# Kernel tuning notes

Measured on AMD Instinct MI355X. Metric: run time of the kernel, lower is better.

## Reference

```python
import jax, jax.numpy as jnp
import numpy as np

B, NQ, S, D = 2, 2048, 2048, 1024
H, HD, OUT = 16, 64, 1024


def setup_inputs() -> dict:
    key = jax.random.key(0)
    ks = jax.random.split(key, 8)
    scale = 1.0 / np.sqrt(D)
    return {
        "queries": jax.random.normal(ks[0], (B, NQ, D), jnp.float32),
        "keys": jax.random.normal(ks[1], (B, S, D), jnp.float32),
        "values": jax.random.normal(ks[2], (B, S, D), jnp.float32),
        "indicators": jax.random.uniform(ks[3], (B, S), jnp.float32),
        "Wq": jax.random.normal(ks[4], (D, H * HD), jnp.float32) * scale,
        "Wk": jax.random.normal(ks[5], (D, H * HD), jnp.float32) * scale,
        "Wv": jax.random.normal(ks[6], (D, H * HD), jnp.float32) * scale,
        "Wo": jax.random.normal(ks[7], (H * HD, OUT), jnp.float32) * scale,
    }


def reference(queries, keys, values, indicators, Wq, Wk, Wv, Wo):
    b, nq, _ = queries.shape
    s = keys.shape[1]
    # projections -> [b, len, H, HD] -> [b, H, len, HD]
    Q = (queries @ Wq).reshape(b, nq, H, HD).transpose(0, 2, 1, 3)
    K = (keys @ Wk).reshape(b, s, H, HD).transpose(0, 2, 1, 3)
    V = (values @ Wv).reshape(b, s, H, HD).transpose(0, 2, 1, 3)
    # scores [b, H, nq, s], softmax over s, THEN multiplicative mask
    scores = jnp.einsum("bhqd,bhkd->bhqk", Q, K) / jnp.sqrt(jnp.float32(HD))
    probs = jax.nn.softmax(scores, axis=-1)
    probs = probs * indicators[:, None, None, :]  # post-softmax mask
    ctx = jnp.einsum("bhqk,bhkd->bhqd", probs, V)
    ctx = ctx.transpose(0, 2, 1, 3).reshape(b, nq, H * HD)
    return ctx @ Wo
```

## Files before the change

kernel.cpp:

```cpp
#include <hip/hip_runtime.h>


typedef float f32x4 __attribute__((ext_vector_type(4)));
typedef __bf16 bf16x8 __attribute__((ext_vector_type(8)));
typedef __bf16 bf16x4 __attribute__((ext_vector_type(4)));

#define DEVINL __device__ __forceinline__

DEVINL void gll16(const void* g, void* l) {
  __builtin_amdgcn_global_load_lds((const __attribute__((address_space(1))) void*)g,
                                   (__attribute__((address_space(3))) void*)l, 16, 0, 0);
}
DEVINL bf16x8 ldfrag(const void* p) { return __builtin_bit_cast(bf16x8, *(const int4*)p); }
DEVINL f32x4 mfma16(bf16x8 a, bf16x8 b, f32x4 c) {
  return __builtin_amdgcn_mfma_f32_16x16x32_bf16(a, b, c, 0, 0, 0);
}
DEVINL unsigned cvtpk(float a, float b) {
  union {
    __bf16 h[2];
    unsigned u;
  } r;
  r.h[0] = (__bf16)a;
  r.h[1] = (__bf16)b;
  return r.u;
}
DEVINL void swap32(unsigned& a, unsigned& b) {
  asm("v_permlane32_swap_b32 %0, %1" : "+v"(a), "+v"(b));
}
DEVINL void swap16(unsigned& a, unsigned& b) {
  asm("v_permlane16_swap_b32 %0, %1" : "+v"(a), "+v"(b));
}

__global__ __launch_bounds__(256) void prep_k(
    const float* __restrict__ q, const float* __restrict__ k,
    const float* __restrict__ v, const float* __restrict__ Wq,
    const float* __restrict__ Wk, const float* __restrict__ Wv,
    const float* __restrict__ Wo, __bf16* __restrict__ qo, __bf16* __restrict__ ko,
    __bf16* __restrict__ vo, __bf16* __restrict__ o0, __bf16* __restrict__ o1,
    __bf16* __restrict__ o2, __bf16* __restrict__ o3) {
  const int bid = blockIdx.x;
  const int t = threadIdx.x;
  if (bid < 12288) {
    int plane = bid >> 12, bx = bid & 4095;
    const float* s = plane == 0 ? q : (plane == 1 ? k : v);
    __bf16* d = plane == 0 ? qo : (plane == 1 ? ko : vo);
    size_t i = ((size_t)bx * 256 + t) * 4;
    float4 f = *(const float4*)(s + i);
    bf16x4 o = {(__bf16)f.x, (__bf16)f.y, (__bf16)f.z, (__bf16)f.w};
    *(bf16x4*)(d + i) = o;
  } else {
    __shared__ float tl[32][33];
    int wid = bid - 12288;
    int z = wid >> 10, x = wid & 31, y = (wid >> 5) & 31;
    const float* W = z == 0 ? Wq : z == 1 ? Wk : z == 2 ? Wv : Wo;
    __bf16* o = z == 0 ? o0 : z == 1 ? o1 : z == 2 ? o2 : o3;
    float scale = z == 0 ? 0.125f * 1.44269504f : 1.0f;
    int c0 = x * 32, r0 = y * 32;
    int tx = t & 31, ty = t >> 5;
#pragma unroll
    for (int rr = 0; rr < 32; rr += 8)
      tl[rr + ty][tx] = W[(size_t)(r0 + rr + ty) * 1024 + c0 + tx];
    __syncthreads();
#pragma unroll
    for (int cc = 0; cc < 32; cc += 8)
      o[(size_t)(c0 + cc + ty) * 1024 + r0 + tx] = (__bf16)(tl[tx][cc + ty] * scale);
  }
}

template <int MT>
DEVINL void gemm_core(const __bf16* __restrict__ A, const __bf16* __restrict__ Bt,
                      int K, int m0, int n0, char* As, char* Bs, f32x4 (&acc)[MT][4],
                      int t) {
  const int lane = t & 63, wv = t >> 6;
  const int li = lane & 15, g = lane >> 4;
  const int wr = wv >> 1, wc = wv & 1;
  const size_t lda = (size_t)K * 2;
  for (int kt = 0; kt < K; kt += 32) {
    if (kt) __syncthreads();
#pragma unroll
    for (int p = 0; p < MT / 2; ++p) {
      int off = p * 4096 + t * 16;
      int row = off >> 6, ch = (off >> 4) & 3;
      int gch = ch ^ ((row >> 1) & 3);
      gll16((const char*)A + (size_t)(m0 + row) * lda + (size_t)kt * 2 + gch * 16,
            As + off);
    }
#pragma unroll
    for (int p = 0; p < 2; ++p) {
      int off = p * 4096 + t * 16;
      int row = off >> 6, ch = (off >> 4) & 3;
      int gch = ch ^ ((row >> 1) & 3);
      gll16((const char*)Bt + (size_t)(n0 + row) * lda + (size_t)kt * 2 + gch * 16,
            Bs + off);
    }
    __syncthreads();
    bf16x8 af[MT], bfr[4];
#pragma unroll
    for (int mt = 0; mt < MT; ++mt) {
      int row = wr * (MT * 16) + mt * 16 + li;
      int gch = g ^ ((row >> 1) & 3);
      af[mt] = ldfrag(As + row * 64 + gch * 16);
    }
#pragma unroll
    for (int nt = 0; nt < 4; ++nt) {
      int row = wc * 64 + nt * 16 + li;
      int gch = g ^ ((row >> 1) & 3);
      bfr[nt] = ldfrag(Bs + row * 64 + gch * 16);
    }
#pragma unroll
    for (int mt = 0; mt < MT; ++mt)
#pragma unroll
      for (int nt = 0; nt < 4; ++nt)
        acc[mt][nt] = mfma16(af[mt], bfr[nt], acc[mt][nt]);
  }
}

__global__ __launch_bounds__(256) void gemm_qkv(
    const __bf16* __restrict__ qb, const __bf16* __restrict__ kb,
    const __bf16* __restrict__ vb, const __bf16* __restrict__ WqT,
    const __bf16* __restrict__ WkT, const __bf16* __restrict__ WvT,
    const float* __restrict__ ind, __bf16* __restrict__ Qp, __bf16* __restrict__ Kp,
    __bf16* __restrict__ Vtp) {
  __shared__ __align__(16) char As[4 * 2048];
  __shared__ __align__(16) char Bs[8192];
  const int z = blockIdx.z;
  const __bf16* A = z == 0 ? qb : z == 1 ? kb : vb;
  const __bf16* Bt = z == 0 ? WqT : z == 1 ? WkT : WvT;
  const int m0 = blockIdx.y * 128, n0 = blockIdx.x * 128;
  f32x4 acc[4][4] = {};
  gemm_core<4>(A, Bt, 1024, m0, n0, As, Bs, acc, threadIdx.x);
  const int lane = threadIdx.x & 63, wv = threadIdx.x >> 6;
  const int li = lane & 15, g = lane >> 4;
  const int wr = wv >> 1, wc = wv & 1;
#pragma unroll
  for (int mt = 0; mt < 4; ++mt)
#pragma unroll
    for (int nt = 0; nt < 4; ++nt) {
      int m = m0 + wr * 64 + mt * 16 + g * 4;
      int n = n0 + wc * 64 + nt * 16 + li;
      if (z < 2) {
        __bf16* Cb = z ? Kp : Qp;
#pragma unroll
        for (int r = 0; r < 4; ++r)
          Cb[(size_t)(m + r) * 1024 + n] = (__bf16)acc[mt][nt][r];
      } else {
        float4 i4 = *(const float4*)(ind + m);
        bf16x4 o = {(__bf16)(acc[mt][nt][0] * i4.x), (__bf16)(acc[mt][nt][1] * i4.y),
                    (__bf16)(acc[mt][nt][2] * i4.z), (__bf16)(acc[mt][nt][3] * i4.w)};
        *(bf16x4*)(Vtp + (size_t)n * 4096 + m) = o;
      }
    }
}

__global__ __launch_bounds__(256) void gemm_out(const __bf16* __restrict__ ctx,
                                                const __bf16* __restrict__ WoT,
                                                float* __restrict__ out) {
  __shared__ __align__(16) char As[2 * 2048];
  __shared__ __align__(16) char Bs[8192];
  const int m0 = blockIdx.y * 64, n0 = blockIdx.x * 128;
  f32x4 acc[2][4] = {};
  gemm_core<2>(ctx, WoT, 1024, m0, n0, As, Bs, acc, threadIdx.x);
  const int lane = threadIdx.x & 63, wv = threadIdx.x >> 6;
  const int li = lane & 15, g = lane >> 4;
  const int wr = wv >> 1, wc = wv & 1;
#pragma unroll
  for (int mt = 0; mt < 2; ++mt)
#pragma unroll
    for (int nt = 0; nt < 4; ++nt) {
      int m = m0 + wr * 32 + mt * 16 + g * 4;
      int n = n0 + wc * 64 + nt * 16 + li;
#pragma unroll
      for (int r = 0; r < 4; ++r) out[(size_t)(m + r) * 1024 + n] = acc[mt][nt][r];
    }
}

__global__ __launch_bounds__(256) void flash_k(
    const __bf16* __restrict__ Qp, const __bf16* __restrict__ Kp,
    const __bf16* __restrict__ Vt, __bf16* __restrict__ ctx0,
    __bf16* __restrict__ ctx1, __bf16* __restrict__ ctx2, float* __restrict__ pl) {
  __shared__ __align__(16) char smem[16384];
  char* kv = smem;
  const int t = threadIdx.x;
  const int lane = t & 63, wv = t >> 6;
  const int li = lane & 15, g = lane >> 4;
  const int sp = blockIdx.x >> 9, rest = blockIdx.x & 511;
  const int qt = rest & 15, h = (rest >> 4) & 15, b = rest >> 8;
  const int kt0 = (sp * 32) / 3, kt1 = (sp * 32 + 32) / 3;
  const size_t qrow0 = (size_t)b * 2048 + (size_t)qt * 128;
  __bf16* ctx = sp == 0 ? ctx0 : (sp == 1 ? ctx1 : ctx2);

#pragma unroll
  for (int p = 0; p < 4; ++p) {
    int off = p * 4096 + t * 16;
    int row = off >> 7, ch = (off >> 4) & 7;
    int gch = ch ^ (row & 7);
    gll16((const char*)Qp + ((qrow0 + row) * 1024 + h * 64) * 2 + gch * 16, smem + off);
  }
  __syncthreads();

  bf16x8 qf[2][2];
#pragma unroll
  for (int nt = 0; nt < 2; ++nt)
#pragma unroll
    for (int ks = 0; ks < 2; ++ks) {
      int row = wv * 32 + nt * 16 + li;
      int gch = (4 * ks + g) ^ (row & 7);
      qf[nt][ks] = ldfrag(smem + row * 128 + gch * 16);
    }

  f32x4 acc[4][2] = {};
  float lsum[2] = {0.0f, 0.0f};

  for (int kt = kt0; kt < kt1; ++kt) {
    __syncthreads();
#pragma unroll
    for (int p = 0; p < 2; ++p) {
      int off = p * 4096 + t * 16;
      int row = off >> 7, ch = (off >> 4) & 7;
      int gch = ch ^ (row & 7);
      gll16((const char*)Kp +
                (((size_t)b * 2048 + kt * 64 + row) * 1024 + h * 64) * 2 + gch * 16,
            kv + off);
      gll16((const char*)Vt +
                ((size_t)(h * 64 + row) * 4096 + (size_t)b * 2048 + kt * 64) * 2 +
                gch * 16,
            kv + 8192 + off);
    }
    __syncthreads();

    unsigned pk[4][2][2];
#pragma unroll
    for (int mt = 0; mt < 4; ++mt) {
      f32x4 st0 = {}, st1 = {};
      int row = mt * 16 + li;
#pragma unroll
      for (int ks = 0; ks < 2; ++ks) {
        int gch = (4 * ks + g) ^ (row & 7);
        bf16x8 kf = ldfrag(kv + row * 128 + gch * 16);
        st0 = mfma16(kf, qf[0][ks], st0);
        st1 = mfma16(kf, qf[1][ks], st1);
      }
      float p0 = __builtin_amdgcn_exp2f(st0[0]);
      float p1 = __builtin_amdgcn_exp2f(st0[1]);
      float p2 = __builtin_amdgcn_exp2f(st0[2]);
      float p3 = __builtin_amdgcn_exp2f(st0[3]);
      lsum[0] += (p0 + p1) + (p2 + p3);
      pk[mt][0][0] = cvtpk(p0, p1);
      pk[mt][0][1] = cvtpk(p2, p3);
      p0 = __builtin_amdgcn_exp2f(st1[0]);
      p1 = __builtin_amdgcn_exp2f(st1[1]);
      p2 = __builtin_amdgcn_exp2f(st1[2]);
      p3 = __builtin_amdgcn_exp2f(st1[3]);
      lsum[1] += (p0 + p1) + (p2 + p3);
      pk[mt][1][0] = cvtpk(p0, p1);
      pk[mt][1][1] = cvtpk(p2, p3);
    }

#pragma unroll
    for (int kc = 0; kc < 2; ++kc) {
      unsigned a00 = pk[2 * kc][0][0], b00 = pk[2 * kc + 1][0][0];
      unsigned a01 = pk[2 * kc][0][1], b01 = pk[2 * kc + 1][0][1];
      unsigned a10 = pk[2 * kc][1][0], b10 = pk[2 * kc + 1][1][0];
      unsigned a11 = pk[2 * kc][1][1], b11 = pk[2 * kc + 1][1][1];
      swap32(a00, b00);
      swap16(a00, b00);
      swap32(a01, b01);
      swap16(a01, b01);
      swap32(a10, b10);
      swap16(a10, b10);
      swap32(a11, b11);
      swap16(a11, b11);
      uint4 u0 = {a00, a01, b00, b01};
      uint4 u1 = {a10, a11, b10, b11};
      bf16x8 pf0 = __builtin_bit_cast(bf16x8, u0);
      bf16x8 pf1 = __builtin_bit_cast(bf16x8, u1);
#pragma unroll
      for (int mtd = 0; mtd < 4; ++mtd) {
        int row = mtd * 16 + li;
        int gch = (4 * kc + g) ^ (row & 7);
        bf16x8 vf = ldfrag(kv + 8192 + row * 128 + gch * 16);
        acc[mtd][0] = mfma16(vf, pf0, acc[mtd][0]);
        acc[mtd][1] = mfma16(vf, pf1, acc[mtd][1]);
      }
    }
  }

#pragma unroll
  for (int nt = 0; nt < 2; ++nt) {
    float l = lsum[nt];
    l += __shfl_xor(l, 16);
    l += __shfl_xor(l, 32);
    float linv = 1.0f / l;
    size_t qrow = qrow0 + wv * 32 + nt * 16 + li;
    if (g == 0) pl[((size_t)sp * 4096 + qrow) * 16 + h] = l;
#pragma unroll
    for (int mtd = 0; mtd < 4; ++mtd) {
      bf16x4 o = {(__bf16)(acc[mtd][nt][0] * linv), (__bf16)(acc[mtd][nt][1] * linv),
                  (__bf16)(acc[mtd][nt][2] * linv), (__bf16)(acc[mtd][nt][3] * linv)};
      *(bf16x4*)(ctx + qrow * 1024 + h * 64 + mtd * 16 + g * 4) = o;
    }
  }
}

__global__ __launch_bounds__(256) void combine_k(const __bf16* __restrict__ c0,
                                                 const __bf16* __restrict__ c1,
                                                 const __bf16* __restrict__ c2,
                                                 const float* __restrict__ pl,
                                                 __bf16* __restrict__ ctx) {
  size_t e = ((size_t)blockIdx.x * 256 + threadIdx.x) * 8;
  int qrow = (int)(e >> 10), h = ((int)e & 1023) >> 6;
  float l0 = pl[(size_t)qrow * 16 + h];
  float l1 = pl[(size_t)(4096 + qrow) * 16 + h];
  float l2 = pl[(size_t)(8192 + qrow) * 16 + h];
  float w = 1.0f / (l0 + l1 + l2);
  float w0 = l0 * w, w1 = l1 * w, w2 = l2 * w;
  bf16x8 a = *(const bf16x8*)(c0 + e);
  bf16x8 b = *(const bf16x8*)(c1 + e);
  bf16x8 c = *(const bf16x8*)(c2 + e);
  bf16x8 o;
#pragma unroll
  for (int i = 0; i < 8; ++i)
    o[i] = (__bf16)((float)a[i] * w0 + (float)b[i] * w1 + (float)c[i] * w2);
  *(bf16x8*)(ctx + e) = o;
}

extern "C" void kernel_launch(void* const* d_in, const int* in_sizes, int n_in,
                              void* d_out, int out_size, void* d_ws, size_t ws_size,
                              hipStream_t stream) {
  const float* q = (const float*)d_in[0];
  const float* k = (const float*)d_in[1];
  const float* v = (const float*)d_in[2];
  const float* ind = (const float*)d_in[3];
  const float* Wq = (const float*)d_in[4];
  const float* Wk = (const float*)d_in[5];
  const float* Wv = (const float*)d_in[6];
  const float* Wo = (const float*)d_in[7];
  char* ws = (char*)d_ws;
  const size_t MB = 1024 * 1024;
  __bf16* qb = (__bf16*)(ws + 0);
  __bf16* kb = (__bf16*)(ws + 8 * MB);
  __bf16* vb = (__bf16*)(ws + 16 * MB);
  __bf16* WqT = (__bf16*)(ws + 24 * MB);
  __bf16* WkT = (__bf16*)(ws + 26 * MB);
  __bf16* WvT = (__bf16*)(ws + 28 * MB);
  __bf16* WoT = (__bf16*)(ws + 30 * MB);
  __bf16* Qp = (__bf16*)(ws + 32 * MB);
  __bf16* Kp = (__bf16*)(ws + 40 * MB);
  __bf16* Vtp = (__bf16*)(ws + 48 * MB);
  __bf16* ctx0 = (__bf16*)(ws + 0);
  __bf16* ctx1 = (__bf16*)(ws + 8 * MB);
  __bf16* ctx2 = (__bf16*)(ws + 16 * MB);
  float* pl = (float*)(ws + 24 * MB);
  __bf16* ctx = (__bf16*)(ws + 48 * MB);
  float* out = (float*)d_out;

  prep_k<<<dim3(16384), 256, 0, stream>>>(q, k, v, Wq, Wk, Wv, Wo, qb, kb, vb, WqT,
                                          WkT, WvT, WoT);
  gemm_qkv<<<dim3(8, 32, 3), 256, 0, stream>>>(qb, kb, vb, WqT, WkT, WvT, ind, Qp, Kp,
                                               Vtp);
  flash_k<<<dim3(1536), 256, 0, stream>>>(Qp, Kp, Vtp, ctx0, ctx1, ctx2, pl);
  combine_k<<<dim3(2048), 256, 0, stream>>>(ctx0, ctx1, ctx2, pl, ctx);
  gemm_out<<<dim3(8, 64), 256, 0, stream>>>(ctx, WoT, out);
}
```

Measured before the change: 228.2 us.

## Double-buffer K tiles and split K/V waits in flash attention loop

Restructures the flash attention inner loop so the next K tile is prefetched into a second LDS buffer while the current one is consumed. V loads are issued at the start of each iteration and waited on only before the PV MFMAs, using explicit vmcnt waits and raw barriers instead of __syncthreads. It also raises wave priority around the MFMA sections. The aim is to hide global-to-LDS latency behind the QK and softmax compute, at the cost of 8KB more LDS and fragile hand-counted waitcnt ordering.

```diff
diff --git a/kernel.cpp b/kernel.cpp
--- a/kernel.cpp
+++ b/kernel.cpp
@@ -30,6 +30,11 @@
 DEVINL void swap16(unsigned& a, unsigned& b) {
   asm("v_permlane16_swap_b32 %0, %1" : "+v"(a), "+v"(b));
 }
+
+#define SBAR() __builtin_amdgcn_s_barrier()
+#define SCHED0() __builtin_amdgcn_sched_barrier(0)
+#define WAITV(n) asm volatile("s_waitcnt vmcnt(" #n ")" ::: "memory")
+#define WAITL0() asm volatile("s_waitcnt lgkmcnt(0)" ::: "memory")
 
 __global__ __launch_bounds__(256) void prep_k(
     const float* __restrict__ q, const float* __restrict__ k,
@@ -178,14 +183,15 @@
     const __bf16* __restrict__ Qp, const __bf16* __restrict__ Kp,
     const __bf16* __restrict__ Vt, __bf16* __restrict__ ctx0,
     __bf16* __restrict__ ctx1, __bf16* __restrict__ ctx2, float* __restrict__ pl) {
-  __shared__ __align__(16) char smem[16384];
-  char* kv = smem;
+  __shared__ __align__(16) char smem[24576];
+  char* vbuf = smem + 16384;
   const int t = threadIdx.x;
   const int lane = t & 63, wv = t >> 6;
   const int li = lane & 15, g = lane >> 4;
   const int sp = blockIdx.x >> 9, rest = blockIdx.x & 511;
   const int qt = rest & 15, h = (rest >> 4) & 15, b = rest >> 8;
   const int kt0 = (sp * 32) / 3, kt1 = (sp * 32 + 32) / 3;
+  const int ntile = kt1 - kt0;
   const size_t qrow0 = (size_t)b * 2048 + (size_t)qt * 128;
   __bf16* ctx = sp == 0 ? ctx0 : (sp == 1 ? ctx1 : ctx2);
 
@@ -194,9 +200,21 @@
     int off = p * 4096 + t * 16;
     int row = off >> 7, ch = (off >> 4) & 7;
     int gch = ch ^ (row & 7);
-    gll16((const char*)Qp + ((qrow0 + row) * 1024 + h * 64) * 2 + gch * 16, smem + off);
-  }
-  __syncthreads();
+    gll16((const char*)Qp + ((qrow0 + row) * 1024 + h * 64) * 2 + gch * 16,
+          smem + 8192 + off);
+  }
+#pragma unroll
+  for (int p = 0; p < 2; ++p) {
+    int off = p * 4096 + t * 16;
+    int row = off >> 7, ch = (off >> 4) & 7;
+    int gch = ch ^ (row & 7);
+    gll16((const char*)Kp +
+              (((size_t)b * 2048 + kt0 * 64 + row) * 1024 + h * 64) * 2 + gch * 16,
+          smem + off);
+  }
+  WAITV(2);
+  SBAR();
+  SCHED0();
 
   bf16x8 qf[2][2];
 #pragma unroll
@@ -205,30 +223,50 @@
     for (int ks = 0; ks < 2; ++ks) {
       int row = wv * 32 + nt * 16 + li;
       int gch = (4 * ks + g) ^ (row & 7);
-      qf[nt][ks] = ldfrag(smem + row * 128 + gch * 16);
-    }
+      qf[nt][ks] = ldfrag(smem + 8192 + row * 128 + gch * 16);
+    }
+  SCHED0();
+  WAITL0();
+  SBAR();
+  SCHED0();
 
   f32x4 acc[4][2] = {};
   float lsum[2] = {0.0f, 0.0f};
 
-  for (int kt = kt0; kt < kt1; ++kt) {
-    __syncthreads();
+  for (int t_ = 0; t_ < ntile; ++t_) {
+    const int kt = kt0 + t_;
+    char* kbuf = smem + (t_ & 1) * 8192;
 #pragma unroll
     for (int p = 0; p < 2; ++p) {
       int off = p * 4096 + t * 16;
       int row = off >> 7, ch = (off >> 4) & 7;
       int gch = ch ^ (row & 7);
-      gll16((const char*)Kp +
-                (((size_t)b * 2048 + kt * 64 + row) * 1024 + h * 64) * 2 + gch * 16,
-            kv + off);
       gll16((const char*)Vt +
                 ((size_t)(h * 64 + row) * 4096 + (size_t)b * 2048 + kt * 64) * 2 +
                 gch * 16,
-            kv + 8192 + off);
-    }
-    __syncthreads();
+            vbuf + off);
+    }
+    if (t_ + 1 < ntile) {
+      char* knxt = smem + ((t_ + 1) & 1) * 8192;
+#pragma unroll
+      for (int p = 0; p < 2; ++p) {
+        int off = p * 4096 + t * 16;
+        int row = off >> 7, ch = (off >> 4) & 7;
+        int gch = ch ^ (row & 7);
+        gll16((const char*)Kp +
+                  (((size_t)b * 2048 + (kt + 1) * 64 + row) * 1024 + h * 64) * 2 +
+                  gch * 16,
+              knxt + off);
+      }
+      WAITV(4);
+    } else {
+      WAITV(2);
+    }
+    SBAR();
+    SCHED0();
 
     unsigned pk[4][2][2];
+    __builtin_amdgcn_s_setprio(1);
 #pragma unroll
     for (int mt = 0; mt < 4; ++mt) {
       f32x4 st0 = {}, st1 = {};
@@ -236,7 +274,7 @@
 #pragma unroll
       for (int ks = 0; ks < 2; ++ks) {
         int gch = (4 * ks + g) ^ (row & 7);
-        bf16x8 kf = ldfrag(kv + row * 128 + gch * 16);
+        bf16x8 kf = ldfrag(kbuf + row * 128 + gch * 16);
         st0 = mfma16(kf, qf[0][ks], st0);
         st1 = mfma16(kf, qf[1][ks], st1);
       }
@@ -255,7 +293,18 @@
       pk[mt][1][0] = cvtpk(p0, p1);
       pk[mt][1][1] = cvtpk(p2, p3);
     }
-
+    __builtin_amdgcn_s_setprio(0);
+
+    SCHED0();
+    if (t_ + 1 < ntile) {
+      WAITV(2);
+    } else {
+      WAITV(0);
+    }
+    SBAR();
+    SCHED0();
+
+    __builtin_amdgcn_s_setprio(1);
 #pragma unroll
     for (int kc = 0; kc < 2; ++kc) {
       unsigned a00 = pk[2 * kc][0][0], b00 = pk[2 * kc + 1][0][0];
@@ -278,11 +327,17 @@
       for (int mtd = 0; mtd < 4; ++mtd) {
         int row = mtd * 16 + li;
         int gch = (4 * kc + g) ^ (row & 7);
-        bf16x8 vf = ldfrag(kv + 8192 + row * 128 + gch * 16);
+        bf16x8 vf = ldfrag(vbuf + row * 128 + gch * 16);
         acc[mtd][0] = mfma16(vf, pf0, acc[mtd][0]);
         acc[mtd][1] = mfma16(vf, pf1, acc[mtd][1]);
       }
     }
+    __builtin_amdgcn_s_setprio(0);
+
+    SCHED0();
+    WAITL0();
+    SBAR();
+    SCHED0();
   }
 
 #pragma unroll
```

Result: no change. 230.7 us (+1.1%).

## Stage transposed V output through LDS and remap GEMM block order

Applied to the files above, without the earlier changes.

The V projection epilogue now writes its masked bf16 tile into a padded shared-memory buffer and then emits coalesced 16-byte rows to the transposed Vt layout, replacing scattered 8-byte stores. Both the QKV and output GEMMs also remap the linear block index so consecutive blocks walk differently over M/N tiles, intended to spread work across XCDs and improve cache reuse. The shared buffer grows to about 34KB, which may reduce occupancy, and extra barriers are added in the V path.

```diff
diff --git a/kernel.cpp b/kernel.cpp
--- a/kernel.cpp
+++ b/kernel.cpp
@@ -121,35 +121,56 @@
     const __bf16* __restrict__ WkT, const __bf16* __restrict__ WvT,
     const float* __restrict__ ind, __bf16* __restrict__ Qp, __bf16* __restrict__ Kp,
     __bf16* __restrict__ Vtp) {
-  __shared__ __align__(16) char As[4 * 2048];
-  __shared__ __align__(16) char Bs[8192];
+  __shared__ __align__(16) char shm[34816];
+  char* As = shm;
+  char* Bs = shm + 8192;
   const int z = blockIdx.z;
   const __bf16* A = z == 0 ? qb : z == 1 ? kb : vb;
   const __bf16* Bt = z == 0 ? WqT : z == 1 ? WkT : WvT;
-  const int m0 = blockIdx.y * 128, n0 = blockIdx.x * 128;
+  const int lin = blockIdx.x + (int)blockIdx.y * 8;
+  const int w = (lin & 7) * 32 + (lin >> 3);
+  const int m0 = (w >> 3) * 128, n0 = (w & 7) * 128;
   f32x4 acc[4][4] = {};
   gemm_core<4>(A, Bt, 1024, m0, n0, As, Bs, acc, threadIdx.x);
   const int lane = threadIdx.x & 63, wv = threadIdx.x >> 6;
   const int li = lane & 15, g = lane >> 4;
   const int wr = wv >> 1, wc = wv & 1;
-#pragma unroll
-  for (int mt = 0; mt < 4; ++mt)
-#pragma unroll
-    for (int nt = 0; nt < 4; ++nt) {
-      int m = m0 + wr * 64 + mt * 16 + g * 4;
-      int n = n0 + wc * 64 + nt * 16 + li;
-      if (z < 2) {
-        __bf16* Cb = z ? Kp : Qp;
+  if (z < 2) {
+    __bf16* Cb = z ? Kp : Qp;
+#pragma unroll
+    for (int mt = 0; mt < 4; ++mt)
+#pragma unroll
+      for (int nt = 0; nt < 4; ++nt) {
+        int m = m0 + wr * 64 + mt * 16 + g * 4;
+        int n = n0 + wc * 64 + nt * 16 + li;
 #pragma unroll
         for (int r = 0; r < 4; ++r)
           Cb[(size_t)(m + r) * 1024 + n] = (__bf16)acc[mt][nt][r];
-      } else {
+      }
+  } else {
+    __syncthreads();
+    __bf16(*T)[136] = (__bf16(*)[136])shm;
+#pragma unroll
+    for (int mt = 0; mt < 4; ++mt)
+#pragma unroll
+      for (int nt = 0; nt < 4; ++nt) {
+        int m = m0 + wr * 64 + mt * 16 + g * 4;
+        int n_l = wc * 64 + nt * 16 + li;
         float4 i4 = *(const float4*)(ind + m);
         bf16x4 o = {(__bf16)(acc[mt][nt][0] * i4.x), (__bf16)(acc[mt][nt][1] * i4.y),
                     (__bf16)(acc[mt][nt][2] * i4.z), (__bf16)(acc[mt][nt][3] * i4.w)};
-        *(bf16x4*)(Vtp + (size_t)n * 4096 + m) = o;
+        *(bf16x4*)&T[n_l][wr * 64 + mt * 16 + g * 4] = o;
       }
-    }
+    __syncthreads();
+    const int tt = threadIdx.x;
+#pragma unroll
+    for (int pass = 0; pass < 8; ++pass) {
+      int n_l = pass * 16 + (tt >> 4);
+      int mc = (tt & 15) * 8;
+      int4 val = *(const int4*)&T[n_l][mc];
+      *(int4*)(Vtp + (size_t)(n0 + n_l) * 4096 + m0 + mc) = val;
+    }
+  }
 }
 
 __global__ __launch_bounds__(256) void gemm_out(const __bf16* __restrict__ ctx,
@@ -157,7 +178,9 @@
                                                 float* __restrict__ out) {
   __shared__ __align__(16) char As[2 * 2048];
   __shared__ __align__(16) char Bs[8192];
-  const int m0 = blockIdx.y * 64, n0 = blockIdx.x * 128;
+  const int lin = blockIdx.x + (int)blockIdx.y * 8;
+  const int w = (lin & 7) * 64 + (lin >> 3);
+  const int m0 = (w >> 3) * 64, n0 = (w & 7) * 128;
   f32x4 acc[2][4] = {};
   gemm_core<2>(ctx, WoT, 1024, m0, n0, As, Bs, acc, threadIdx.x);
   const int lane = threadIdx.x & 63, wv = threadIdx.x >> 6;
```

After: 233.6 us. 1.02x slower.

## Fuse split-KV combine into output projection GEMM A-tile load

Applied to the files above, without the earlier changes.

Removes the separate combine kernel and instead merges the three partial flash-attention context buffers, weighted by their softmax sums, while loading the A tile inside the output GEMM. This eliminates one launch and the write and re-read of the combined context buffer. In exchange, each column block of the output GEMM re-reads all three partial buffers and recomputes the weights. The A loads become synchronous register loads rather than async global-to-LDS copies.

```diff
diff --git a/kernel.cpp b/kernel.cpp
--- a/kernel.cpp
+++ b/kernel.cpp
@@ -152,17 +152,70 @@
     }
 }
 
-__global__ __launch_bounds__(256) void gemm_out(const __bf16* __restrict__ ctx,
-                                                const __bf16* __restrict__ WoT,
-                                                float* __restrict__ out) {
-  __shared__ __align__(16) char As[2 * 2048];
+__global__ __launch_bounds__(256) void gemm_out(
+    const __bf16* __restrict__ c0, const __bf16* __restrict__ c1,
+    const __bf16* __restrict__ c2, const float* __restrict__ pl,
+    const __bf16* __restrict__ WoT, float* __restrict__ out) {
+  __shared__ __align__(16) char As[4096];
   __shared__ __align__(16) char Bs[8192];
-  const int m0 = blockIdx.y * 64, n0 = blockIdx.x * 128;
-  f32x4 acc[2][4] = {};
-  gemm_core<2>(ctx, WoT, 1024, m0, n0, As, Bs, acc, threadIdx.x);
-  const int lane = threadIdx.x & 63, wv = threadIdx.x >> 6;
+  const int t = threadIdx.x;
+  const int lane = t & 63, wv = t >> 6;
   const int li = lane & 15, g = lane >> 4;
   const int wr = wv >> 1, wc = wv & 1;
+  const int m0 = blockIdx.y * 64, n0 = blockIdx.x * 128;
+  const int arow = t >> 2;
+  const int agch = (t & 3) ^ ((arow >> 1) & 3);
+  const size_t abase = (size_t)(m0 + arow) * 1024 + agch * 8;
+  const float* plr = pl + (size_t)(m0 + arow) * 16;
+  f32x4 acc[2][4] = {};
+  for (int kt = 0; kt < 32; ++kt) {
+    if (kt) __syncthreads();
+    {
+      const int h = kt >> 1;
+      float l0 = plr[h], l1 = plr[65536 + h], l2 = plr[131072 + h];
+      float w = 1.0f / (l0 + l1 + l2);
+      float w0 = l0 * w, w1 = l1 * w, w2 = l2 * w;
+      bf16x8 a = *(const bf16x8*)(c0 + abase + kt * 32);
+      bf16x8 b = *(const bf16x8*)(c1 + abase + kt * 32);
+      bf16x8 c = *(const bf16x8*)(c2 + abase + kt * 32);
+      unsigned ow[4];
+#pragma unroll
+      for (int i = 0; i < 4; ++i) {
+        float e0 = (float)a[2 * i] * w0 + (float)b[2 * i] * w1 + (float)c[2 * i] * w2;
+        float e1 = (float)a[2 * i + 1] * w0 + (float)b[2 * i + 1] * w1 +
+                   (float)c[2 * i + 1] * w2;
+        ow[i] = cvtpk(e0, e1);
+      }
+      *(int4*)(As + t * 16) = (int4){(int)ow[0], (int)ow[1], (int)ow[2], (int)ow[3]};
+    }
+#pragma unroll
+    for (int p = 0; p < 2; ++p) {
+      int off = p * 4096 + t * 16;
+      int row = off >> 6, ch = (off >> 4) & 3;
+      int gch = ch ^ ((row >> 1) & 3);
+      gll16((const char*)WoT + (size_t)(n0 + row) * 2048 + (size_t)kt * 64 + gch * 16,
+            Bs + off);
+    }
+    __syncthreads();
+    bf16x8 af[2], bfr[4];
+#pragma unroll
+    for (int mt = 0; mt < 2; ++mt) {
+      int row = wr * 32 + mt * 16 + li;
+      int gch = g ^ ((row >> 1) & 3);
+      af[mt] = ldfrag(As + row * 64 + gch * 16);
+    }
+#pragma unroll
+    for (int nt = 0; nt < 4; ++nt) {
+      int row = wc * 64 + nt * 16 + li;
+      int gch = g ^ ((row >> 1) & 3);
+      bfr[nt] = ldfrag(Bs + row * 64 + gch * 16);
+    }
+#pragma unroll
+    for (int mt = 0; mt < 2; ++mt)
+#pragma unroll
+      for (int nt = 0; nt < 4; ++nt)
+        acc[mt][nt] = mfma16(af[mt], bfr[nt], acc[mt][nt]);
+  }
 #pragma unroll
   for (int mt = 0; mt < 2; ++mt)
 #pragma unroll
@@ -300,28 +353,6 @@
       *(bf16x4*)(ctx + qrow * 1024 + h * 64 + mtd * 16 + g * 4) = o;
     }
   }
-}
-
-__global__ __launch_bounds__(256) void combine_k(const __bf16* __restrict__ c0,
-                                                 const __bf16* __restrict__ c1,
-                                                 const __bf16* __restrict__ c2,
-                                                 const float* __restrict__ pl,
-                                                 __bf16* __restrict__ ctx) {
-  size_t e = ((size_t)blockIdx.x * 256 + threadIdx.x) * 8;
-  int qrow = (int)(e >> 10), h = ((int)e & 1023) >> 6;
-  float l0 = pl[(size_t)qrow * 16 + h];
-  float l1 = pl[(size_t)(4096 + qrow) * 16 + h];
-  float l2 = pl[(size_t)(8192 + qrow) * 16 + h];
-  float w = 1.0f / (l0 + l1 + l2);
-  float w0 = l0 * w, w1 = l1 * w, w2 = l2 * w;
-  bf16x8 a = *(const bf16x8*)(c0 + e);
-  bf16x8 b = *(const bf16x8*)(c1 + e);
-  bf16x8 c = *(const bf16x8*)(c2 + e);
-  bf16x8 o;
-#pragma unroll
-  for (int i = 0; i < 8; ++i)
-    o[i] = (__bf16)((float)a[i] * w0 + (float)b[i] * w1 + (float)c[i] * w2);
-  *(bf16x8*)(ctx + e) = o;
 }
 
 extern "C" void kernel_launch(void* const* d_in, const int* in_sizes, int n_in,
@@ -351,7 +382,6 @@
   __bf16* ctx1 = (__bf16*)(ws + 8 * MB);
   __bf16* ctx2 = (__bf16*)(ws + 16 * MB);
   float* pl = (float*)(ws + 24 * MB);
-  __bf16* ctx = (__bf16*)(ws + 48 * MB);
   float* out = (float*)d_out;
 
   prep_k<<<dim3(16384), 256, 0, stream>>>(q, k, v, Wq, Wk, Wv, Wo, qb, kb, vb, WqT,
@@ -359,6 +389,5 @@
   gemm_qkv<<<dim3(8, 32, 3), 256, 0, stream>>>(qb, kb, vb, WqT, WkT, WvT, ind, Qp, Kp,
                                                Vtp);
   flash_k<<<dim3(1536), 256, 0, stream>>>(Qp, Kp, Vtp, ctx0, ctx1, ctx2, pl);
-  combine_k<<<dim3(2048), 256, 0, stream>>>(ctx0, ctx1, ctx2, pl, ctx);
-  gemm_out<<<dim3(8, 64), 256, 0, stream>>>(ctx, WoT, out);
-}
+  gemm_out<<<dim3(8, 64), 256, 0, stream>>>(ctx0, ctx1, ctx2, pl, WoT, out);
+}
```

Result: slower. 238.8 us (+4.7%).
